# Kernel tuning notes

Hardware: AMD Instinct MI355X
Metric: run time of the kernel (lower is better)

## Reference

```python
import jax, jax.numpy as jnp
import numpy as np

N_NODES = 10000
N_EDGES = 160000
F_IN, D1, D2, D_OUT, K = 512, 512, 512, 256, 3


def _gcn_layer(x, row, col, w, W, b, n):
    # PyG GCNConv (improved=False): add self-loops with weight 1, sym norm.
    loop = jnp.arange(n)
    r = jnp.concatenate([row, loop])
    c = jnp.concatenate([col, loop])
    ww = jnp.concatenate([w, jnp.ones((n,), w.dtype)])
    deg = jax.ops.segment_sum(ww, c, num_segments=n)
    dinv = jnp.where(deg > 0, jax.lax.rsqrt(deg), 0.0)
    norm = dinv[r] * ww * dinv[c]              # [E+N]
    h = x @ W                                  # dense GEMM first (as PyG lin)
    out = jax.ops.segment_sum(norm[:, None] * h[r], c, num_segments=n)
    return out + b


def _cheb_layer(x, row, col, w, Wk, b, n):
    # PyG ChebConv, normalization='sym', lambda_max=2.0:
    # L_hat = 2L/lmax - I = -D^{-1/2} A D^{-1/2} (self-loops removed first).
    w0 = jnp.where(row == col, jnp.zeros((), w.dtype), w)  # remove self loops
    deg = jax.ops.segment_sum(w0, row, num_segments=n)
    dinv = jnp.where(deg > 0, jax.lax.rsqrt(deg), 0.0)
    norm = dinv[row] * w0 * dinv[col]          # [E]

    def lhat(z):  # L_hat @ z
        return -jax.ops.segment_sum(norm[:, None] * z[row], col, num_segments=n)

    Tx0 = x
    out = Tx0 @ Wk[0]
    Tx1 = lhat(x)
    out = out + Tx1 @ Wk[1]
    for k in range(2, Wk.shape[0]):            # static K, fine to unroll
        Tx2 = 2.0 * lhat(Tx1) - Tx0
        out = out + Tx2 @ Wk[k]
        Tx0, Tx1 = Tx1, Tx2
    return out + b


def setup_inputs() -> dict:
    key = jax.random.key(0)
    ks = jax.random.split(key, 9)
    x = jax.random.normal(ks[0], (N_NODES, F_IN), dtype=jnp.float32)
    edge_index = jax.random.randint(ks[1], (2, N_EDGES), 0, N_NODES, dtype=jnp.int64)
    edge_weight = jax.random.uniform(ks[2], (N_EDGES,), dtype=jnp.float32)
    s = lambda fan: 1.0 / np.sqrt(fan)
    W1 = jax.random.normal(ks[3], (F_IN, D1), dtype=jnp.float32) * s(F_IN)
    b1 = jnp.zeros((D1,), jnp.float32)
    W2 = jax.random.normal(ks[4], (D1, D2), dtype=jnp.float32) * s(D1)
    b2 = jnp.zeros((D2,), jnp.float32)
    Wc = jax.random.normal(ks[5], (K, D2, D_OUT), dtype=jnp.float32) * s(D2)
    bc = jnp.zeros((D_OUT,), jnp.float32)
    return {"x": x, "edge_index": edge_index, "edge_weight": edge_weight,
            "W1": W1, "b1": b1, "W2": W2, "b2": b2, "Wc": Wc, "bc": bc}


def reference(x, edge_index, edge_weight, W1, b1, W2, b2, Wc, bc):
    row, col = edge_index[0], edge_index[1]
    n = x.shape[0]
    h = jax.nn.celu(_gcn_layer(x, row, col, edge_weight, W1, b1, n))
    h = jax.nn.celu(_gcn_layer(h, row, col, edge_weight, W2, b2, n))
    h = jax.nn.celu(_cheb_layer(h, row, col, edge_weight, Wc, bc, n))
    return h
```

## Files before the change

### kernel.cpp

```cpp
#include <hip/hip_runtime.h>
#include <math.h>

#define N_NODES 10000
#define N_EDGES 160000
#define FDIM    512
#define DOUT    256
#define NCAT    768

typedef unsigned short ushort_t;
typedef unsigned int   uint_t;
typedef __attribute__((ext_vector_type(8))) short bf16x8;
typedef __attribute__((ext_vector_type(4))) float f32x4;

__device__ inline ushort_t f2bf(float f) {
    uint_t u = __float_as_uint(f);
    u += 0x7fffu + ((u >> 16) & 1u);
    return (ushort_t)(u >> 16);
}
__device__ inline void bf2f8(uint4 u, float* v) {
    v[0] = __uint_as_float(u.x << 16); v[1] = __uint_as_float(u.x & 0xffff0000u);
    v[2] = __uint_as_float(u.y << 16); v[3] = __uint_as_float(u.y & 0xffff0000u);
    v[4] = __uint_as_float(u.z << 16); v[5] = __uint_as_float(u.z & 0xffff0000u);
    v[6] = __uint_as_float(u.w << 16); v[7] = __uint_as_float(u.w & 0xffff0000u);
}
__device__ inline uint4 f2bf8v(const float* v) {
    uint4 u;
    u.x = (uint_t)f2bf(v[0]) | ((uint_t)f2bf(v[1]) << 16);
    u.y = (uint_t)f2bf(v[2]) | ((uint_t)f2bf(v[3]) << 16);
    u.z = (uint_t)f2bf(v[4]) | ((uint_t)f2bf(v[5]) << 16);
    u.w = (uint_t)f2bf(v[6]) | ((uint_t)f2bf(v[7]) << 16);
    return u;
}
__device__ inline void gld_lds16(const ushort_t* g, ushort_t* l) {
    __builtin_amdgcn_global_load_lds(
        (const __attribute__((address_space(1))) unsigned int*)g,
        (__attribute__((address_space(3))) unsigned int*)l,
        16, 0, 0);
}

#define EDGE_BLOCKS 625
#define XB_BLOCKS   5000

__global__ __launch_bounds__(256) void k_pre1(
    const int* __restrict__ row, const int* __restrict__ col,
    const float* __restrict__ w,
    float* deg_g, float* deg_c, int* counts,
    const float* __restrict__ x,  ushort_t* __restrict__ xb,
    const float* __restrict__ W1, ushort_t* __restrict__ W1t,
    const float* __restrict__ W2, ushort_t* __restrict__ W2t,
    const float* __restrict__ Wc, ushort_t* __restrict__ Wcatt)
{
    __shared__ float tile[64][65];
    int b = blockIdx.x;
    int tid = threadIdx.x;
    if (b < EDGE_BLOCKS) {
        int e = b * 256 + tid;
        if (e < N_EDGES) {
            int r = row[e], c = col[e];
            float wv = w[e];
            atomicAdd(&deg_g[c], wv);
            if (r != c) atomicAdd(&deg_c[r], wv);
            atomicAdd(&counts[c], 1);
        }
        return;
    }
    b -= EDGE_BLOCKS;
    if (b < XB_BLOCKS) {
        int t = b * 256 + tid;
        float4 v = *(const float4*)(x + (size_t)t * 4);
        uint2 p;
        p.x = (uint_t)f2bf(v.x) | ((uint_t)f2bf(v.y) << 16);
        p.y = (uint_t)f2bf(v.z) | ((uint_t)f2bf(v.w) << 16);
        *(uint2*)(xb + (size_t)t * 4) = p;
        return;
    }
    b -= XB_BLOCKS;
    const float* src; const float* src2 = nullptr;
    ushort_t* dst; int kt, ntG, srcld;
    if (b < 64) {
        kt = b >> 3; ntG = b & 7; srcld = FDIM;
        src = W1 + (size_t)(kt * 64) * FDIM + ntG * 64;
        dst = W1t;
    } else if (b < 128) {
        int bb = b - 64;
        kt = bb >> 3; ntG = bb & 7; srcld = FDIM;
        src = W2 + (size_t)(kt * 64) * FDIM + ntG * 64;
        dst = W2t;
    } else {
        int bb = b - 128;
        ntG = bb / 8; kt = bb % 8; srcld = DOUT;
        int s = ntG >> 2;
        int nl = (ntG & 3) * 64;
        if (s == 0) {
            src  = Wc + (size_t)(kt * 64) * DOUT + nl;
            src2 = Wc + (size_t)2 * FDIM * DOUT + (size_t)(kt * 64) * DOUT + nl;
        } else if (s == 1) {
            src  = Wc + (size_t)1 * FDIM * DOUT + (size_t)(kt * 64) * DOUT + nl;
        } else {
            src  = Wc + (size_t)2 * FDIM * DOUT + (size_t)(kt * 64) * DOUT + nl;
        }
        dst = Wcatt;
    }
    {
        int r = tid >> 2, c0 = (tid & 3) * 16;
        const float* sp = src + (size_t)r * srcld + c0;
#pragma unroll
        for (int q = 0; q < 4; ++q) {
            float4 a = *(const float4*)(sp + q * 4);
            if (src2) {
                float4 bsub = *(const float4*)(src2 + (size_t)r * srcld + c0 + q * 4);
                a.x -= bsub.x; a.y -= bsub.y; a.z -= bsub.z; a.w -= bsub.w;
            }
            tile[r][c0 + q * 4 + 0] = a.x;
            tile[r][c0 + q * 4 + 1] = a.y;
            tile[r][c0 + q * 4 + 2] = a.z;
            tile[r][c0 + q * 4 + 3] = a.w;
        }
    }
    __syncthreads();
    {
        int n = tid >> 2, k0 = (tid & 3) * 16;
        float v[16];
#pragma unroll
        for (int i = 0; i < 16; ++i) v[i] = tile[k0 + i][n];
        uint4 u0 = f2bf8v(v);
        uint4 u1 = f2bf8v(v + 8);
        ushort_t* dp = dst + (size_t)(ntG * 64 + n) * FDIM + kt * 64 + k0;
        *(uint4*)dp = u0;
        *(uint4*)(dp + 8) = u1;
    }
}

__global__ __launch_bounds__(256) void k_dinv_scan1(
    const float* __restrict__ deg_g, const float* __restrict__ deg_c,
    float* __restrict__ dinv_g, float* __restrict__ dinv_c,
    const int* __restrict__ counts, int* __restrict__ rp,
    int* __restrict__ part, int n)
{
    __shared__ int s[256];
    int tid = threadIdx.x;
    int i = blockIdx.x * 256 + tid;
    if (i < n) {
        dinv_g[i] = rsqrtf(deg_g[i] + 1.0f);
        float d = deg_c[i];
        dinv_c[i] = d > 0.f ? rsqrtf(d) : 0.f;
    }
    int v = (i < n) ? counts[i] : 0;
    s[tid] = v;
    __syncthreads();
    for (int o = 1; o < 256; o <<= 1) {
        int t = (tid >= o) ? s[tid - o] : 0;
        __syncthreads();
        s[tid] += t;
        __syncthreads();
    }
    if (i < n) rp[i] = s[tid] - v;
    if (tid == 255) part[blockIdx.x] = s[255];
}

__global__ __launch_bounds__(256) void k_scan23(int* __restrict__ rp,
                                                const int* __restrict__ part,
                                                int nb, int n) {
    __shared__ int soff[64];
    __shared__ int stot;
    int tid = threadIdx.x;
    if (tid < 64) {
        int v = (tid < nb) ? part[tid] : 0;
        int x = v;
        for (int o = 1; o < 64; o <<= 1) {
            int y = __shfl_up(x, o, 64);
            if (tid >= o) x += y;
        }
        soff[tid] = x - v;
        if (tid == 63) stot = x;
    }
    __syncthreads();
    int i = blockIdx.x * 256 + tid;
    if (i < n) rp[i] += soff[blockIdx.x];
    if (blockIdx.x == 0 && tid == 0) rp[n] = stot;
}

__global__ void k_fill(const int* __restrict__ row, const int* __restrict__ col,
                       const float* __restrict__ w,
                       const float* __restrict__ dinv_g, const float* __restrict__ dinv_c,
                       const int* __restrict__ rp, int* __restrict__ fill,
                       int2* __restrict__ eg, int2* __restrict__ ec, int E) {
    int e = blockIdx.x * blockDim.x + threadIdx.x;
    if (e >= E) return;
    int r = row[e], c = col[e];
    float wv = w[e];
    float ng = dinv_g[r] * wv * dinv_g[c];
    float w0 = (r == c) ? 0.f : wv;
    float nc = -(dinv_c[r] * w0 * dinv_c[c]);
    int pos = rp[c] + atomicAdd(&fill[c], 1);
    eg[pos] = make_int2(r, __float_as_int(ng));
    ec[pos] = make_int2(r, __float_as_int(nc));
}

__global__ __launch_bounds__(256) void k_mgemm(
    const ushort_t* __restrict__ A, int lda,
    const ushort_t* __restrict__ Bt, int ldb,
    int M, int K, int N, int nbx, int nby,
    ushort_t* __restrict__ outB)
{
    __shared__ ushort_t As[64 * 32];
    __shared__ ushort_t Bs[128 * 32];

    int id = blockIdx.x;
    int j = id & 7, t = id >> 3;
    int by = t % nby;
    int bx = (t / nby) * 8 + j;
    if (bx >= nbx) return;

    const int tid  = threadIdx.x;
    const int w    = tid >> 6;
    const int lane = tid & 63;
    const int l15  = lane & 15;
    const int quad = lane >> 4;
    const int bm = bx * 64, bn = by * 128;
    const int wm = (w & 1) * 32;
    const int wn = (w >> 1) * 64;

    const int sr = lane >> 2;
    const int sc = (lane & 3) * 8;
    int arow = min(bm + w * 16 + sr, M - 1);
    const ushort_t* ag = A + (size_t)arow * lda + sc;
    ushort_t* al = As + (w * 16 + sr) * 32 + sc;
    const ushort_t* bg0 = Bt + (size_t)(bn + w * 32 + sr) * ldb + sc;
    const ushort_t* bg1 = bg0 + (size_t)16 * ldb;
    ushort_t* bl0 = Bs + (w * 32 + sr) * 32 + sc;
    ushort_t* bl1 = bl0 + 16 * 32;

    f32x4 acc[2][4] = {};

    for (int k0 = 0; k0 < K; k0 += 32) {
        __syncthreads();
        gld_lds16(ag + k0, al);
        gld_lds16(bg0 + k0, bl0);
        gld_lds16(bg1 + k0, bl1);
        __syncthreads();
        bf16x8 af[2], bfr[4];
#pragma unroll
        for (int i = 0; i < 2; ++i)
            af[i] = *(const bf16x8*)(As + (wm + i * 16 + l15) * 32 + quad * 8);
#pragma unroll
        for (int jj = 0; jj < 4; ++jj)
            bfr[jj] = *(const bf16x8*)(Bs + (wn + jj * 16 + l15) * 32 + quad * 8);
#pragma unroll
        for (int i = 0; i < 2; ++i)
#pragma unroll
            for (int jj = 0; jj < 4; ++jj)
                acc[i][jj] = __builtin_amdgcn_mfma_f32_16x16x32_bf16(af[i], bfr[jj], acc[i][jj], 0, 0, 0);
    }

#pragma unroll
    for (int i = 0; i < 2; ++i) {
        int rowb = bm + wm + i * 16 + quad * 4;
#pragma unroll
        for (int jj = 0; jj < 4; ++jj) {
            int col = bn + wn + jj * 16 + l15;
#pragma unroll
            for (int r = 0; r < 4; ++r) {
                int rr = rowb + r;
                if (rr < M)
                    outB[(size_t)rr * N + col] = f2bf(acc[i][jj][r]);
            }
        }
    }
}

template<int SL>
__global__ __launch_bounds__(256) void k_sagg(
    const ushort_t* __restrict__ h, int hs, int hoff,
    const int2* __restrict__ er, const int* __restrict__ rp,
    const float* __restrict__ dinv_g,
    const ushort_t* __restrict__ other, int os, int ooff, float sB,
    const float* __restrict__ bias, float sA,
    ushort_t* __restrict__ outB, float* __restrict__ outF, int outs, int celu)
{
    const int id  = blockIdx.x;
    const int sl  = id % SL;
    const int tid = threadIdx.x;
    const int c   = (id / SL) * 32 + (tid >> 3);
    if (c >= N_NODES) return;
    const int f = sl * 64 + ((tid & 7) << 3);
    const ushort_t* hp = h + hoff + f;

    float acc[8] = {0.f, 0.f, 0.f, 0.f, 0.f, 0.f, 0.f, 0.f};
    int e = rp[c];
    const int e1 = rp[c + 1];
    for (; e + 4 <= e1; e += 4) {
        int2 p0 = er[e], p1 = er[e + 1], p2 = er[e + 2], p3 = er[e + 3];
        uint4 u0 = *(const uint4*)(hp + (size_t)p0.x * hs);
        uint4 u1 = *(const uint4*)(hp + (size_t)p1.x * hs);
        uint4 u2 = *(const uint4*)(hp + (size_t)p2.x * hs);
        uint4 u3 = *(const uint4*)(hp + (size_t)p3.x * hs);
        float n0 = __int_as_float(p0.y), n1 = __int_as_float(p1.y);
        float n2 = __int_as_float(p2.y), n3 = __int_as_float(p3.y);
        float v0[8], v1[8], v2[8], v3[8];
        bf2f8(u0, v0); bf2f8(u1, v1); bf2f8(u2, v2); bf2f8(u3, v3);
#pragma unroll
        for (int i = 0; i < 8; ++i) {
            acc[i] = fmaf(n0, v0[i], acc[i]);
            acc[i] = fmaf(n1, v1[i], acc[i]);
            acc[i] = fmaf(n2, v2[i], acc[i]);
            acc[i] = fmaf(n3, v3[i], acc[i]);
        }
    }
    for (; e < e1; ++e) {
        int2 p = er[e];
        uint4 u = *(const uint4*)(hp + (size_t)p.x * hs);
        float nv = __int_as_float(p.y);
        float v[8]; bf2f8(u, v);
#pragma unroll
        for (int i = 0; i < 8; ++i) acc[i] = fmaf(nv, v[i], acc[i]);
    }

    if (dinv_g) {
        float dv = dinv_g[c];
        float d2 = dv * dv;
        uint4 u = *(const uint4*)(hp + (size_t)c * hs);
        float v[8]; bf2f8(u, v);
#pragma unroll
        for (int i = 0; i < 8; ++i) acc[i] = fmaf(d2, v[i], acc[i]);
    }
    float r[8];
#pragma unroll
    for (int i = 0; i < 8; ++i) r[i] = sA * acc[i];
    if (other) {
        uint4 u = *(const uint4*)(other + (size_t)c * os + ooff + f);
        float o[8]; bf2f8(u, o);
#pragma unroll
        for (int i = 0; i < 8; ++i) r[i] = fmaf(sB, o[i], r[i]);
    }
    if (bias) {
#pragma unroll
        for (int i = 0; i < 8; ++i) r[i] += bias[f + i];
    }
    if (celu) {
#pragma unroll
        for (int i = 0; i < 8; ++i) r[i] = r[i] > 0.f ? r[i] : expm1f(r[i]);
    }
    if (outF) {
        float* op = outF + (size_t)c * outs + f;
        *(float4*)op       = make_float4(r[0], r[1], r[2], r[3]);
        *(float4*)(op + 4) = make_float4(r[4], r[5], r[6], r[7]);
    } else {
        *(uint4*)(outB + (size_t)c * outs + f) = f2bf8v(r);
    }
}


extern "C" void kernel_launch(void* const* d_in, const int* in_sizes, int n_in,
                              void* d_out, int out_size, void* d_ws, size_t ws_size,
                              hipStream_t stream) {
    const float* x  = (const float*)d_in[0];
    const int*   ei = (const int*)d_in[1];
    const float* ew = (const float*)d_in[2];
    const float* W1 = (const float*)d_in[3];
    const float* b1 = (const float*)d_in[4];
    const float* W2 = (const float*)d_in[5];
    const float* b2 = (const float*)d_in[6];
    const float* Wc = (const float*)d_in[7];
    const float* bc = (const float*)d_in[8];
    float* out = (float*)d_out;

    const int* row = ei;
    const int* col = ei + N_EDGES;

    char* ws = (char*)d_ws;
    size_t off = 0;
    auto alloc = [&](size_t bytes) -> void* {
        void* p = ws + off;
        off += (bytes + 255) & ~(size_t)255;
        return p;
    };
    ushort_t* xb    = (ushort_t*)alloc((size_t)N_NODES * FDIM * 2);
    ushort_t* bufA  = (ushort_t*)alloc((size_t)N_NODES * FDIM * 2);
    ushort_t* bufB  = (ushort_t*)alloc((size_t)N_NODES * FDIM * 2);
    ushort_t* Y     = (ushort_t*)alloc((size_t)N_NODES * NCAT * 2);
    ushort_t* P     = (ushort_t*)alloc((size_t)N_NODES * DOUT * 2);
    ushort_t* W1t   = (ushort_t*)alloc((size_t)FDIM * FDIM * 2);
    ushort_t* W2t   = (ushort_t*)alloc((size_t)FDIM * FDIM * 2);
    ushort_t* Wcatt = (ushort_t*)alloc((size_t)NCAT * FDIM * 2);
    size_t zs = off;
    float* deg_g  = (float*)alloc((size_t)N_NODES * 4);
    float* deg_c  = (float*)alloc((size_t)N_NODES * 4);
    int*   counts = (int*)alloc((size_t)N_NODES * 4);
    int*   fillb  = (int*)alloc((size_t)N_NODES * 4);
    size_t ze = off;
    float* dinv_g = (float*)alloc((size_t)N_NODES * 4);
    float* dinv_c = (float*)alloc((size_t)N_NODES * 4);
    int*   rp     = (int*)alloc((size_t)(N_NODES + 1) * 4);
    int*   part   = (int*)alloc(64 * 4);
    int2*  eg     = (int2*)alloc((size_t)N_EDGES * 8);
    int2*  ec     = (int2*)alloc((size_t)N_EDGES * 8);

    const int TB = 256;
    dim3 edgeGrid((N_EDGES + TB - 1) / TB);
    int nScanB = (N_NODES + 255) / 256;

    hipMemsetAsync(ws + zs, 0, ze - zs, stream);
    k_pre1<<<EDGE_BLOCKS + XB_BLOCKS + 224, 256, 0, stream>>>(
        row, col, ew, deg_g, deg_c, counts,
        x, xb, W1, W1t, W2, W2t, Wc, Wcatt);
    k_dinv_scan1<<<nScanB, 256, 0, stream>>>(deg_g, deg_c, dinv_g, dinv_c, counts, rp, part, N_NODES);
    k_scan23<<<nScanB, 256, 0, stream>>>(rp, part, nScanB, N_NODES);
    k_fill<<<edgeGrid, TB, 0, stream>>>(row, col, ew, dinv_g, dinv_c, rp, fillb, eg, ec, N_EDGES);

    auto mgemm = [&](const ushort_t* A, const ushort_t* Bt, int N, ushort_t* oB) {
        int nbx = (N_NODES + 63) / 64, nby = N / 128;
        int G = 8 * (((nbx + 7) / 8) * nby);
        k_mgemm<<<G, 256, 0, stream>>>(A, FDIM, Bt, FDIM, N_NODES, FDIM, N, nbx, nby, oB);
    };
    int g8 = ((N_NODES + 31) / 32) * 8;
    int g4 = ((N_NODES + 31) / 32) * 4;

    mgemm(xb, W1t, FDIM, bufA);
    k_sagg<8><<<g8, 256, 0, stream>>>(bufA, FDIM, 0, eg, rp, dinv_g,
                                      (const ushort_t*)nullptr, 0, 0, 0.f,
                                      b1, 1.f, bufB, (float*)nullptr, FDIM, 1);
    mgemm(bufB, W2t, FDIM, bufA);
    k_sagg<8><<<g8, 256, 0, stream>>>(bufA, FDIM, 0, eg, rp, dinv_g,
                                      (const ushort_t*)nullptr, 0, 0, 0.f,
                                      b2, 1.f, bufB, (float*)nullptr, FDIM, 1);
    mgemm(bufB, Wcatt, NCAT, Y);
    k_sagg<4><<<g4, 256, 0, stream>>>(Y, NCAT, 2 * DOUT, ec, rp,
                                      (const float*)nullptr,
                                      Y, NCAT, DOUT, 1.f,
                                      (const float*)nullptr, 2.f,
                                      P, (float*)nullptr, DOUT, 0);
    k_sagg<4><<<g4, 256, 0, stream>>>(P, DOUT, 0, ec, rp,
                                      (const float*)nullptr,
                                      Y, NCAT, 0, 1.f,
                                      bc, 1.f,
                                      (ushort_t*)nullptr, out, DOUT, 1);
}
```

Baseline: 239.7 us.

## Fuse edge fill with first GEMM, sort aggregation nodes by degree, deepen GEMM k-step

Merges the CSR fill kernel and the first GEMM into one launch, and adds a degree histogram whose per-node scatter builds a permutation. The aggregation kernels then process nodes grouped by degree to balance load across warps. The GEMM now loads two 32-wide k-slices per barrier, halving sync count. Weight transposes use smaller 32x32 tiles with more blocks. It adds indirection through perm in aggregation, which costs some locality in output writes, and adds extra atomics on a small 64-entry histogram.

```diff
diff --git a/kernel.cpp b/kernel.cpp
--- a/kernel.cpp
+++ b/kernel.cpp
@@ -6,6 +6,14 @@
 #define FDIM    512
 #define DOUT    256
 #define NCAT    768
+
+#define EDGE_BLOCKS 625
+#define XB_BLOCKS   5000
+#define TT_BLOCKS   896
+#define NSCANB      40
+#define FILL_BLKS   632
+#define SCAT_BLKS   40
+#define GEMM1_VB    640
 
 typedef unsigned short ushort_t;
 typedef unsigned int   uint_t;
@@ -38,30 +46,25 @@
         16, 0, 0);
 }
 
-#define EDGE_BLOCKS 625
-#define XB_BLOCKS   5000
-
 __global__ __launch_bounds__(256) void k_pre1(
     const int* __restrict__ row, const int* __restrict__ col,
-    const float* __restrict__ w,
+    const float* __restrict__ ew,
     float* deg_g, float* deg_c, int* counts,
     const float* __restrict__ x,  ushort_t* __restrict__ xb,
     const float* __restrict__ W1, ushort_t* __restrict__ W1t,
     const float* __restrict__ W2, ushort_t* __restrict__ W2t,
     const float* __restrict__ Wc, ushort_t* __restrict__ Wcatt)
 {
-    __shared__ float tile[64][65];
+    __shared__ float tile[32][33];
     int b = blockIdx.x;
     int tid = threadIdx.x;
     if (b < EDGE_BLOCKS) {
         int e = b * 256 + tid;
-        if (e < N_EDGES) {
-            int r = row[e], c = col[e];
-            float wv = w[e];
-            atomicAdd(&deg_g[c], wv);
-            if (r != c) atomicAdd(&deg_c[r], wv);
-            atomicAdd(&counts[c], 1);
-        }
+        int r = row[e], c = col[e];
+        float wv = ew[e];
+        atomicAdd(&deg_g[c], wv);
+        if (r != c) atomicAdd(&deg_c[r], wv);
+        atomicAdd(&counts[c], 1);
         return;
     }
     b -= EDGE_BLOCKS;
@@ -76,58 +79,51 @@
     }
     b -= XB_BLOCKS;
     const float* src; const float* src2 = nullptr;
-    ushort_t* dst; int kt, ntG, srcld;
-    if (b < 64) {
-        kt = b >> 3; ntG = b & 7; srcld = FDIM;
-        src = W1 + (size_t)(kt * 64) * FDIM + ntG * 64;
-        dst = W1t;
-    } else if (b < 128) {
-        int bb = b - 64;
-        kt = bb >> 3; ntG = bb & 7; srcld = FDIM;
-        src = W2 + (size_t)(kt * 64) * FDIM + ntG * 64;
-        dst = W2t;
+    ushort_t* dst; int kt, nt, srcld, drb;
+    if (b < 256) {
+        kt = b >> 4; nt = b & 15; srcld = FDIM;
+        src = W1 + (size_t)(kt * 32) * FDIM + nt * 32;
+        dst = W1t; drb = nt * 32;
+    } else if (b < 512) {
+        int bb = b - 256;
+        kt = bb >> 4; nt = bb & 15; srcld = FDIM;
+        src = W2 + (size_t)(kt * 32) * FDIM + nt * 32;
+        dst = W2t; drb = nt * 32;
     } else {
-        int bb = b - 128;
-        ntG = bb / 8; kt = bb % 8; srcld = DOUT;
-        int s = ntG >> 2;
-        int nl = (ntG & 3) * 64;
-        if (s == 0) {
-            src  = Wc + (size_t)(kt * 64) * DOUT + nl;
-            src2 = Wc + (size_t)2 * FDIM * DOUT + (size_t)(kt * 64) * DOUT + nl;
-        } else if (s == 1) {
-            src  = Wc + (size_t)1 * FDIM * DOUT + (size_t)(kt * 64) * DOUT + nl;
+        int bb = b - 512;
+        int sec = bb >> 7, tt = bb & 127;
+        kt = tt >> 3; nt = tt & 7; srcld = DOUT;
+        size_t o = (size_t)(kt * 32) * DOUT + nt * 32;
+        if (sec == 0) {
+            src  = Wc + o;
+            src2 = Wc + (size_t)2 * FDIM * DOUT + o;
+        } else if (sec == 1) {
+            src  = Wc + (size_t)1 * FDIM * DOUT + o;
         } else {
-            src  = Wc + (size_t)2 * FDIM * DOUT + (size_t)(kt * 64) * DOUT + nl;
-        }
-        dst = Wcatt;
+            src  = Wc + (size_t)2 * FDIM * DOUT + o;
+        }
+        dst = Wcatt; drb = sec * 256 + nt * 32;
     }
     {
-        int r = tid >> 2, c0 = (tid & 3) * 16;
-        const float* sp = src + (size_t)r * srcld + c0;
-#pragma unroll
-        for (int q = 0; q < 4; ++q) {
-            float4 a = *(const float4*)(sp + q * 4);
-            if (src2) {
-                float4 bsub = *(const float4*)(src2 + (size_t)r * srcld + c0 + q * 4);
-                a.x -= bsub.x; a.y -= bsub.y; a.z -= bsub.z; a.w -= bsub.w;
-            }
-            tile[r][c0 + q * 4 + 0] = a.x;
-            tile[r][c0 + q * 4 + 1] = a.y;
-            tile[r][c0 + q * 4 + 2] = a.z;
-            tile[r][c0 + q * 4 + 3] = a.w;
-        }
+        int r = tid >> 3, c0 = (tid & 7) << 2;
+        float4 av = *(const float4*)(src + (size_t)r * srcld + c0);
+        if (src2) {
+            float4 bs = *(const float4*)(src2 + (size_t)r * srcld + c0);
+            av.x -= bs.x; av.y -= bs.y; av.z -= bs.z; av.w -= bs.w;
+        }
+        tile[r][c0 + 0] = av.x; tile[r][c0 + 1] = av.y;
+        tile[r][c0 + 2] = av.z; tile[r][c0 + 3] = av.w;
     }
     __syncthreads();
     {
-        int n = tid >> 2, k0 = (tid & 3) * 16;
-        float v[16];
-#pragma unroll
-        for (int i = 0; i < 16; ++i) v[i] = tile[k0 + i][n];
-        uint4 u0 = f2bf8v(v);
-        uint4 u1 = f2bf8v(v + 8);
-        ushort_t* dp = dst + (size_t)(ntG * 64 + n) * FDIM + kt * 64 + k0;
-        *(uint4*)dp = u0;
-        *(uint4*)(dp + 8) = u1;
+        int n = tid >> 3, k0 = (tid & 7) << 2;
+        float v[4];
+#pragma unroll
+        for (int i = 0; i < 4; ++i) v[i] = tile[k0 + i][n];
+        uint2 p;
+        p.x = (uint_t)f2bf(v[0]) | ((uint_t)f2bf(v[1]) << 16);
+        p.y = (uint_t)f2bf(v[2]) | ((uint_t)f2bf(v[3]) << 16);
+        *(uint2*)(dst + (size_t)(drb + n) * FDIM + kt * 32 + k0) = p;
     }
 }
 
@@ -135,7 +131,7 @@
     const float* __restrict__ deg_g, const float* __restrict__ deg_c,
     float* __restrict__ dinv_g, float* __restrict__ dinv_c,
     const int* __restrict__ counts, int* __restrict__ rp,
-    int* __restrict__ part, int n)
+    int* __restrict__ part, int* __restrict__ hist, int n)
 {
     __shared__ int s[256];
     int tid = threadIdx.x;
@@ -146,6 +142,7 @@
         dinv_c[i] = d > 0.f ? rsqrtf(d) : 0.f;
     }
     int v = (i < n) ? counts[i] : 0;
+    if (i < n) atomicAdd(&hist[min(v, 63)], 1);
     s[tid] = v;
     __syncthreads();
     for (int o = 1; o < 256; o <<= 1) {
@@ -158,60 +155,50 @@
     if (tid == 255) part[blockIdx.x] = s[255];
 }
 
-__global__ __launch_bounds__(256) void k_scan23(int* __restrict__ rp,
-                                                const int* __restrict__ part,
-                                                int nb, int n) {
-    __shared__ int soff[64];
-    __shared__ int stot;
+__global__ __launch_bounds__(256) void k_scan23(
+    int* __restrict__ rp, const int* __restrict__ part,
+    const int* __restrict__ hist, int* __restrict__ hcur, int n)
+{
+    __shared__ int soff[65];
     int tid = threadIdx.x;
     if (tid < 64) {
-        int v = (tid < nb) ? part[tid] : 0;
+        int v = (tid < NSCANB) ? part[tid] : 0;
         int x = v;
         for (int o = 1; o < 64; o <<= 1) {
             int y = __shfl_up(x, o, 64);
             if (tid >= o) x += y;
         }
         soff[tid] = x - v;
-        if (tid == 63) stot = x;
+        if (tid == 63) soff[64] = x;
+    } else if (tid < 128) {
+        int l = tid - 64;
+        int v = hist[l];
+        int x = v;
+        for (int o = 1; o < 64; o <<= 1) {
+            int y = __shfl_up(x, o, 64);
+            if (l >= o) x += y;
+        }
+        hcur[l] = x - v;
     }
     __syncthreads();
     int i = blockIdx.x * 256 + tid;
     if (i < n) rp[i] += soff[blockIdx.x];
-    if (blockIdx.x == 0 && tid == 0) rp[n] = stot;
-}
-
-__global__ void k_fill(const int* __restrict__ row, const int* __restrict__ col,
-                       const float* __restrict__ w,
-                       const float* __restrict__ dinv_g, const float* __restrict__ dinv_c,
-                       const int* __restrict__ rp, int* __restrict__ fill,
-                       int2* __restrict__ eg, int2* __restrict__ ec, int E) {
-    int e = blockIdx.x * blockDim.x + threadIdx.x;
-    if (e >= E) return;
-    int r = row[e], c = col[e];
-    float wv = w[e];
-    float ng = dinv_g[r] * wv * dinv_g[c];
-    float w0 = (r == c) ? 0.f : wv;
-    float nc = -(dinv_c[r] * w0 * dinv_c[c]);
-    int pos = rp[c] + atomicAdd(&fill[c], 1);
-    eg[pos] = make_int2(r, __float_as_int(ng));
-    ec[pos] = make_int2(r, __float_as_int(nc));
-}
-
-__global__ __launch_bounds__(256) void k_mgemm(
-    const ushort_t* __restrict__ A, int lda,
-    const ushort_t* __restrict__ Bt, int ldb,
-    int M, int K, int N, int nbx, int nby,
-    ushort_t* __restrict__ outB)
-{
-    __shared__ ushort_t As[64 * 32];
-    __shared__ ushort_t Bs[128 * 32];
-
-    int id = blockIdx.x;
-    int j = id & 7, t = id >> 3;
+    if (blockIdx.x == 0 && tid == 0) rp[n] = soff[64];
+}
+
+__device__ __forceinline__ void gemmBody(
+    const ushort_t* __restrict__ A, const ushort_t* __restrict__ Bt,
+    int K, int N, ushort_t* __restrict__ outB, int vb, char* smem)
+{
+    const int nby = N >> 7;
+    const int nbx = (N_NODES + 63) >> 6;
+    int j = vb & 7, t = vb >> 3;
     int by = t % nby;
     int bx = (t / nby) * 8 + j;
     if (bx >= nbx) return;
 
+    ushort_t* As = (ushort_t*)smem;
+    ushort_t* Bs = As + 2 * 64 * 32;
     const int tid  = threadIdx.x;
     const int w    = tid >> 6;
     const int lane = tid & 63;
@@ -220,37 +207,42 @@
     const int bm = bx * 64, bn = by * 128;
     const int wm = (w & 1) * 32;
     const int wn = (w >> 1) * 64;
-
     const int sr = lane >> 2;
     const int sc = (lane & 3) * 8;
-    int arow = min(bm + w * 16 + sr, M - 1);
-    const ushort_t* ag = A + (size_t)arow * lda + sc;
-    ushort_t* al = As + (w * 16 + sr) * 32 + sc;
-    const ushort_t* bg0 = Bt + (size_t)(bn + w * 32 + sr) * ldb + sc;
-    const ushort_t* bg1 = bg0 + (size_t)16 * ldb;
+
+    int arow = min(bm + w * 16 + sr, N_NODES - 1);
+    const ushort_t* ag  = A + (size_t)arow * K + sc;
+    const ushort_t* bg0 = Bt + (size_t)(bn + w * 32 + sr) * K + sc;
+    const ushort_t* bg1 = bg0 + (size_t)16 * K;
+    ushort_t* al  = As + (w * 16 + sr) * 32 + sc;
     ushort_t* bl0 = Bs + (w * 32 + sr) * 32 + sc;
     ushort_t* bl1 = bl0 + 16 * 32;
 
     f32x4 acc[2][4] = {};
-
-    for (int k0 = 0; k0 < K; k0 += 32) {
+    for (int k0 = 0; k0 < K; k0 += 64) {
         __syncthreads();
-        gld_lds16(ag + k0, al);
-        gld_lds16(bg0 + k0, bl0);
-        gld_lds16(bg1 + k0, bl1);
+#pragma unroll
+        for (int tt = 0; tt < 2; ++tt) {
+            gld_lds16(ag  + k0 + tt * 32, al  + tt * 2048);
+            gld_lds16(bg0 + k0 + tt * 32, bl0 + tt * 4096);
+            gld_lds16(bg1 + k0 + tt * 32, bl1 + tt * 4096);
+        }
         __syncthreads();
-        bf16x8 af[2], bfr[4];
-#pragma unroll
-        for (int i = 0; i < 2; ++i)
-            af[i] = *(const bf16x8*)(As + (wm + i * 16 + l15) * 32 + quad * 8);
-#pragma unroll
-        for (int jj = 0; jj < 4; ++jj)
-            bfr[jj] = *(const bf16x8*)(Bs + (wn + jj * 16 + l15) * 32 + quad * 8);
-#pragma unroll
-        for (int i = 0; i < 2; ++i)
+#pragma unroll
+        for (int tt = 0; tt < 2; ++tt) {
+            bf16x8 af[2], bfr[4];
+#pragma unroll
+            for (int i = 0; i < 2; ++i)
+                af[i] = *(const bf16x8*)(As + tt * 2048 + (wm + i * 16 + l15) * 32 + quad * 8);
 #pragma unroll
             for (int jj = 0; jj < 4; ++jj)
-                acc[i][jj] = __builtin_amdgcn_mfma_f32_16x16x32_bf16(af[i], bfr[jj], acc[i][jj], 0, 0, 0);
+                bfr[jj] = *(const bf16x8*)(Bs + tt * 4096 + (wn + jj * 16 + l15) * 32 + quad * 8);
+#pragma unroll
+            for (int i = 0; i < 2; ++i)
+#pragma unroll
+                for (int jj = 0; jj < 4; ++jj)
+                    acc[i][jj] = __builtin_amdgcn_mfma_f32_16x16x32_bf16(af[i], bfr[jj], acc[i][jj], 0, 0, 0);
+        }
     }
 
 #pragma unroll
@@ -262,15 +254,64 @@
 #pragma unroll
             for (int r = 0; r < 4; ++r) {
                 int rr = rowb + r;
-                if (rr < M)
+                if (rr < N_NODES)
                     outB[(size_t)rr * N + col] = f2bf(acc[i][jj][r]);
             }
         }
     }
 }
 
+__global__ __launch_bounds__(256) void k_gemmS(
+    const ushort_t* __restrict__ A, const ushort_t* __restrict__ Bt,
+    int N, ushort_t* __restrict__ outB)
+{
+    __shared__ __align__(16) char smem[24576];
+    gemmBody(A, Bt, FDIM, N, outB, blockIdx.x, smem);
+}
+
+__global__ __launch_bounds__(256) void k_fillgemm(
+    const int* __restrict__ row, const int* __restrict__ col,
+    const float* __restrict__ ew,
+    const float* __restrict__ dinv_g, const float* __restrict__ dinv_c,
+    const int* __restrict__ rp, int* __restrict__ fillb,
+    int2* __restrict__ eg, int2* __restrict__ ec,
+    const int* __restrict__ counts, int* __restrict__ hcur, int* __restrict__ perm,
+    const ushort_t* __restrict__ A, const ushort_t* __restrict__ Bt,
+    ushort_t* __restrict__ outB)
+{
+    __shared__ __align__(16) char smem[24576];
+    int b = blockIdx.x;
+    int tid = threadIdx.x;
+    if (b < FILL_BLKS) {
+        int e = b * 256 + tid;
+        if (e < N_EDGES) {
+            int r = row[e], c = col[e];
+            float wv = ew[e];
+            float ng = dinv_g[r] * wv * dinv_g[c];
+            float w0 = (r == c) ? 0.f : wv;
+            float nc = -(dinv_c[r] * w0 * dinv_c[c]);
+            int pos = rp[c] + atomicAdd(&fillb[c], 1);
+            eg[pos] = make_int2(r, __float_as_int(ng));
+            ec[pos] = make_int2(r, __float_as_int(nc));
+        }
+        return;
+    }
+    b -= FILL_BLKS;
+    if (b < SCAT_BLKS) {
+        int i = b * 256 + tid;
+        if (i < N_NODES) {
+            int d = min(counts[i], 63);
+            int pos = atomicAdd(&hcur[d], 1);
+            perm[pos] = i;
+        }
+        return;
+    }
+    gemmBody(A, Bt, FDIM, FDIM, outB, b - SCAT_BLKS, smem);
+}
+
 template<int SL>
 __global__ __launch_bounds__(256) void k_sagg(
+    const int* __restrict__ perm,
     const ushort_t* __restrict__ h, int hs, int hoff,
     const int2* __restrict__ er, const int* __restrict__ rp,
     const float* __restrict__ dinv_g,
@@ -278,11 +319,12 @@
     const float* __restrict__ bias, float sA,
     ushort_t* __restrict__ outB, float* __restrict__ outF, int outs, int celu)
 {
-    const int id  = blockIdx.x;
-    const int sl  = id % SL;
+    const int vb  = blockIdx.x;
+    const int sl  = vb % SL;
     const int tid = threadIdx.x;
-    const int c   = (id / SL) * 32 + (tid >> 3);
-    if (c >= N_NODES) return;
+    const int idx = (vb / SL) * 32 + (tid >> 3);
+    if (idx >= N_NODES) return;
+    const int c = perm[idx];
     const int f = sl * 64 + ((tid & 7) << 3);
     const ushort_t* hp = h + hoff + f;
 
@@ -364,7 +406,6 @@
     const float* Wc = (const float*)d_in[7];
     const float* bc = (const float*)d_in[8];
     float* out = (float*)d_out;
-
     const int* row = ei;
     const int* col = ei + N_EDGES;
 
@@ -388,49 +429,45 @@
     float* deg_c  = (float*)alloc((size_t)N_NODES * 4);
     int*   counts = (int*)alloc((size_t)N_NODES * 4);
     int*   fillb  = (int*)alloc((size_t)N_NODES * 4);
+    int*   hist   = (int*)alloc(64 * 4);
     size_t ze = off;
     float* dinv_g = (float*)alloc((size_t)N_NODES * 4);
     float* dinv_c = (float*)alloc((size_t)N_NODES * 4);
     int*   rp     = (int*)alloc((size_t)(N_NODES + 1) * 4);
     int*   part   = (int*)alloc(64 * 4);
+    int*   hcur   = (int*)alloc(64 * 4);
+    int*   perm   = (int*)alloc((size_t)N_NODES * 4);
     int2*  eg     = (int2*)alloc((size_t)N_EDGES * 8);
     int2*  ec     = (int2*)alloc((size_t)N_EDGES * 8);
 
-    const int TB = 256;
-    dim3 edgeGrid((N_EDGES + TB - 1) / TB);
-    int nScanB = (N_NODES + 255) / 256;
-
     hipMemsetAsync(ws + zs, 0, ze - zs, stream);
-    k_pre1<<<EDGE_BLOCKS + XB_BLOCKS + 224, 256, 0, stream>>>(
-        row, col, ew, deg_g, deg_c, counts,
-        x, xb, W1, W1t, W2, W2t, Wc, Wcatt);
-    k_dinv_scan1<<<nScanB, 256, 0, stream>>>(deg_g, deg_c, dinv_g, dinv_c, counts, rp, part, N_NODES);
-    k_scan23<<<nScanB, 256, 0, stream>>>(rp, part, nScanB, N_NODES);
-    k_fill<<<edgeGrid, TB, 0, stream>>>(row, col, ew, dinv_g, dinv_c, rp, fillb, eg, ec, N_EDGES);
-
-    auto mgemm = [&](const ushort_t* A, const ushort_t* Bt, int N, ushort_t* oB) {
-        int nbx = (N_NODES + 63) / 64, nby = N / 128;
-        int G = 8 * (((nbx + 7) / 8) * nby);
-        k_mgemm<<<G, 256, 0, stream>>>(A, FDIM, Bt, FDIM, N_NODES, FDIM, N, nbx, nby, oB);
-    };
+    k_pre1<<<EDGE_BLOCKS + XB_BLOCKS + TT_BLOCKS, 256, 0, stream>>>(
+        row, col, ew, deg_g, deg_c, counts, x, xb, W1, W1t, W2, W2t, Wc, Wcatt);
+    k_dinv_scan1<<<NSCANB, 256, 0, stream>>>(deg_g, deg_c, dinv_g, dinv_c,
+                                             counts, rp, part, hist, N_NODES);
+    k_scan23<<<NSCANB, 256, 0, stream>>>(rp, part, hist, hcur, N_NODES);
+
+    k_fillgemm<<<FILL_BLKS + SCAT_BLKS + GEMM1_VB, 256, 0, stream>>>(
+        row, col, ew, dinv_g, dinv_c, rp, fillb, eg, ec,
+        counts, hcur, perm, xb, W1t, bufA);
+
     int g8 = ((N_NODES + 31) / 32) * 8;
     int g4 = ((N_NODES + 31) / 32) * 4;
 
-    mgemm(xb, W1t, FDIM, bufA);
-    k_sagg<8><<<g8, 256, 0, stream>>>(bufA, FDIM, 0, eg, rp, dinv_g,
+    k_sagg<8><<<g8, 256, 0, stream>>>(perm, bufA, FDIM, 0, eg, rp, dinv_g,
                                       (const ushort_t*)nullptr, 0, 0, 0.f,
                                       b1, 1.f, bufB, (float*)nullptr, FDIM, 1);
-    mgemm(bufB, W2t, FDIM, bufA);
-    k_sagg<8><<<g8, 256, 0, stream>>>(bufA, FDIM, 0, eg, rp, dinv_g,
+    k_gemmS<<<GEMM1_VB, 256, 0, stream>>>(bufB, W2t, FDIM, bufA);
+    k_sagg<8><<<g8, 256, 0, stream>>>(perm, bufA, FDIM, 0, eg, rp, dinv_g,
                                       (const ushort_t*)nullptr, 0, 0, 0.f,
                                       b2, 1.f, bufB, (float*)nullptr, FDIM, 1);
-    mgemm(bufB, Wcatt, NCAT, Y);
-    k_sagg<4><<<g4, 256, 0, stream>>>(Y, NCAT, 2 * DOUT, ec, rp,
+    k_gemmS<<<8 * 20 * 6, 256, 0, stream>>>(bufB, Wcatt, NCAT, Y);
+    k_sagg<4><<<g4, 256, 0, stream>>>(perm, Y, NCAT, 2 * DOUT, ec, rp,
                                       (const float*)nullptr,
                                       Y, NCAT, DOUT, 1.f,
                                       (const float*)nullptr, 2.f,
                                       P, (float*)nullptr, DOUT, 0);
-    k_sagg<4><<<g4, 256, 0, stream>>>(P, DOUT, 0, ec, rp,
+    k_sagg<4><<<g4, 256, 0, stream>>>(perm, P, DOUT, 0, ec, rp,
                                       (const float*)nullptr,
                                       Y, NCAT, 0, 1.f,
                                       bc, 1.f,
```

Result: slower. 271.1 us (+13.1%).
